# Kernel optimization log

Hardware: AMD Instinct MI355X
Metric: run time of the kernel (lower is better)

Reference implementation:

```python
import jax, jax.numpy as jnp
import numpy as np

D = 256

def setup_inputs() -> dict:
    key = jax.random.key(0)
    ks = jax.random.split(key, 7)
    B, N = 4, 4096
    s = 1.0 / np.sqrt(D)
    return {
        "x": jax.random.normal(ks[0], (B, D, N), dtype=jnp.float32),
        "Wq": jax.random.normal(ks[1], (D, D), dtype=jnp.float32) * s,
        "bq": jax.random.normal(ks[2], (D,), dtype=jnp.float32) * s,
        "Wk": jax.random.normal(ks[3], (D, D), dtype=jnp.float32) * s,
        "bk": jax.random.normal(ks[4], (D,), dtype=jnp.float32) * s,
        "Wv": jax.random.normal(ks[5], (D, D), dtype=jnp.float32) * s,
        "bv": jax.random.normal(ks[6], (D,), dtype=jnp.float32) * s,
    }


def reference(x, Wq, bq, Wk, bk, Wv, bv):
    # x: (B, D, N) -> xt: (B, N, D)
    xt = jnp.swapaxes(x, 1, 2)
    q = xt @ Wq + bq  # (B, N, D)
    k = xt @ Wk + bk
    v = xt @ Wv + bv
    # full N x N attention, NO 1/sqrt(d) scaling (matches original)
    attn = jnp.einsum("bnd,bmd->bnm", q, k)
    attn = jax.nn.softmax(attn, axis=-1)
    out = jnp.einsum("bnm,bmd->bnd", attn, v)  # (B, N, D)
    return jnp.swapaxes(out, 1, 2)  # (B, D, N)
```

## Files before the change

### kernel.cpp

```cpp
#include <hip/hip_runtime.h>
#include <math.h>

#define Dd 256
#define Nn 4096
#define Bb 4
#define BQ 128
#define BK 128
#define SPLIT 2

typedef _Float16 f16;
typedef _Float16 half8 __attribute__((ext_vector_type(8)));
typedef _Float16 half4 __attribute__((ext_vector_type(4)));
typedef float f32x4 __attribute__((ext_vector_type(4)));

#define LOG2E 1.4426950408889634f

template <int CTRL>
__device__ __forceinline__ float dppf(float x) {
    int r = __builtin_amdgcn_update_dpp(0, __builtin_bit_cast(int, x),
                                        CTRL, 0xF, 0xF, false);
    return __builtin_bit_cast(float, r);
}
__device__ __forceinline__ float red16_max(float x) {
    x = fmaxf(x, dppf<0x128>(x));
    x = fmaxf(x, dppf<0x124>(x));
    x = fmaxf(x, dppf<0x122>(x));
    x = fmaxf(x, dppf<0x121>(x));
    return x;
}
__device__ __forceinline__ float red16_sum(float x) {
    x += dppf<0x128>(x); x += dppf<0x124>(x);
    x += dppf<0x122>(x); x += dppf<0x121>(x);
    return x;
}

__global__ __launch_bounds__(256) void wtrans(
    const float* __restrict__ Wq, const float* __restrict__ Wk,
    const float* __restrict__ Wv, f16* __restrict__ Wt)
{
    __shared__ float ld[64][65];
    const int which = blockIdx.y;
    const float* W = which == 0 ? Wq : (which == 1 ? Wk : Wv);
    const int tr = (blockIdx.x >> 2) * 64;
    const int tc = (blockIdx.x & 3) * 64;
    const int t = threadIdx.x;
    #pragma unroll
    for (int i = 0; i < 16; ++i) {
        int u = t + i * 256, r = u >> 6, c = u & 63;
        ld[r][c] = W[(size_t)(tr + r) * Dd + tc + c];
    }
    __syncthreads();
    f16* Wo = Wt + (size_t)which * Dd * Dd;
    #pragma unroll
    for (int i = 0; i < 16; ++i) {
        int u = t + i * 256, cp = u >> 6, rp = u & 63;
        Wo[(size_t)(tc + cp) * Dd + tr + rp] = (f16)ld[rp][cp];
    }
}

__global__ __launch_bounds__(512, 1) void qkv_fused(
    const float* __restrict__ x, const f16* __restrict__ Wt,
    const float* __restrict__ bq, const float* __restrict__ bk,
    const float* __restrict__ bv,
    f16* __restrict__ Qh, f16* __restrict__ Kh, f16* __restrict__ Vth)
{
    __shared__ __align__(16) f16 Ws[256][264];
    __shared__ float bs3[3][256];
    f16 (*xT)[264] = (f16 (*)[264])&Ws[0][0];

    const int t = threadIdx.x;
    const int wave = t >> 6, lane = t & 63, quad = lane >> 4, l15 = lane & 15;
    const int g = wave & 3;
    const int h = wave >> 2;
    const int n0 = blockIdx.x * 64;
    const int b = blockIdx.y;

    if (t < 256) { bs3[0][t] = bq[t]; bs3[1][t] = bk[t]; bs3[2][t] = bv[t]; }

    const float* xb = x + (size_t)b * Dd * Nn;
    #pragma unroll
    for (int i = 0; i < 8; ++i) {
        int u = t + i * 512, d = u >> 4, nq = (u & 15) * 4;
        float4 v4 = *(const float4*)&xb[(size_t)d * Nn + n0 + nq];
        xT[nq + 0][d] = (f16)v4.x; xT[nq + 1][d] = (f16)v4.y;
        xT[nq + 2][d] = (f16)v4.z; xT[nq + 3][d] = (f16)v4.w;
    }
    __syncthreads();

    half8 a[8];
    #pragma unroll
    for (int c = 0; c < 8; ++c)
        a[c] = *(const half8*)&xT[16 * g + l15][c * 32 + quad * 8];

    const int nrow = n0 + 16 * g + quad * 4;

    for (int which = 0; which < 3; ++which) {
        __syncthreads();

        const f16* Wb = Wt + (size_t)which * Dd * Dd;
        #pragma unroll
        for (int i = 0; i < 16; ++i) {
            int u = t + i * 512;
            int r = u >> 5, c = u & 31;
            *(half8*)&Ws[r][c * 8] = *(const half8*)(Wb + (size_t)r * Dd + c * 8);
        }
        __syncthreads();

        f32x4 acc[8];
        #pragma unroll
        for (int dt = 0; dt < 8; ++dt) acc[dt] = (f32x4){0.f, 0.f, 0.f, 0.f};
        #pragma unroll
        for (int c = 0; c < 8; ++c) {
            #pragma unroll
            for (int dt = 0; dt < 8; ++dt) {
                half8 bfr = *(const half8*)&Ws[h * 128 + dt * 16 + l15][c * 32 + quad * 8];
                acc[dt] = __builtin_amdgcn_mfma_f32_16x16x32_f16(a[c], bfr, acc[dt], 0, 0, 0);
            }
        }

        if (which < 2) {
            f16* O = (which == 0 ? Qh : Kh) + ((size_t)b * Nn + nrow) * Dd;
            #pragma unroll
            for (int dt = 0; dt < 8; ++dt) {
                int col = h * 128 + dt * 16 + l15;
                float bvv = bs3[which][col];
                #pragma unroll
                for (int r = 0; r < 4; ++r)
                    O[(size_t)r * Dd + col] = (f16)(acc[dt][r] + bvv);
            }
        } else {
            f16* O = Vth + (size_t)b * Dd * Nn;
            #pragma unroll
            for (int dt = 0; dt < 8; ++dt) {
                int col = h * 128 + dt * 16 + l15;
                float bvv = bs3[2][col];
                half4 o;
                #pragma unroll
                for (int r = 0; r < 4; ++r) o[r] = (f16)(acc[dt][r] + bvv);
                *(half4*)&O[(size_t)col * Nn + nrow] = o;
            }
        }
    }
}

__global__ __launch_bounds__(512, 2) void attn_mfma(
    const f16* __restrict__ Qh, const f16* __restrict__ Kh,
    const f16* __restrict__ Vth, f16* __restrict__ Opart,
    float* __restrict__ mpart, float* __restrict__ lpart)
{
    __shared__ __align__(16) f16 Ks[2][BK][264];
    __shared__ float alpha_s[8][16];
    __shared__ float l_sh[8][16];

    const int t    = threadIdx.x;
    const int wave = t >> 6, lane = t & 63;
    const int quad = lane >> 4, l15 = lane & 15;
    const int b    = blockIdx.y;
    const int s    = blockIdx.z;
    const int q0   = blockIdx.x * BQ;
    const int qw   = q0 + wave * 16;
    const int kvlen = Nn / SPLIT;
    const int kv0  = s * kvlen;

    half8 qf[8];
    const f16* Qrow = Qh + ((size_t)b * Nn + qw + l15) * Dd + quad * 8;
    #pragma unroll
    for (int c = 0; c < 8; ++c) {
        qf[c] = *(const half8*)(Qrow + c * 32);
        qf[c] = qf[c] * (f16)LOG2E;
    }

    f32x4 acc[16];
    #pragma unroll
    for (int n = 0; n < 16; ++n) acc[n] = (f32x4){0.f, 0.f, 0.f, 0.f};
    f32x4 m4 = {-1e30f, -1e30f, -1e30f, -1e30f};
    f32x4 l4 = {0.f, 0.f, 0.f, 0.f};

    const f16* Kb   = Kh + (size_t)b * Nn * Dd;
    const f16* Vrow = Vth + (size_t)b * Dd * Nn
                    + (size_t)(wave * 32 + l15) * Nn + quad * 8;

    #pragma unroll
    for (int i = 0; i < 8; ++i) {
        int u = t + i * 512;
        int r = u >> 5, c = u & 31;
        *(half8*)&Ks[0][r][c * 8] =
            *(const half8*)(Kb + (size_t)(kv0 + r) * Dd + c * 8);
    }
    __syncthreads();

    int buf = 0;
    for (int k0 = kv0; k0 < kv0 + kvlen; k0 += BK) {
        const int kn = k0 + BK;
        const bool havenext = kn < kv0 + kvlen;
        half8 kreg[8];
        if (havenext) {
            #pragma unroll
            for (int i = 0; i < 8; ++i) {
                int u = t + i * 512;
                int r = u >> 5, c = u & 31;
                kreg[i] = *(const half8*)(Kb + (size_t)(kn + r) * Dd + c * 8);
            }
        }

        half8 vbf[2][4];
        #pragma unroll
        for (int dt = 0; dt < 2; ++dt) {
            #pragma unroll
            for (int cbb = 0; cbb < 4; ++cbb)
                vbf[dt][cbb] = *(const half8*)(Vrow + (size_t)dt * 16 * Nn + k0 + cbb * 32);
        }

        f32x4 S[8];
        #pragma unroll
        for (int cb = 0; cb < 8; ++cb) S[cb] = (f32x4){0.f, 0.f, 0.f, 0.f};
        #pragma unroll
        for (int c = 0; c < 8; ++c) {
            #pragma unroll
            for (int cb = 0; cb < 8; ++cb) {
                half8 kb = *(const half8*)&Ks[buf][cb * 16 + l15][c * 32 + quad * 8];
                S[cb] = __builtin_amdgcn_mfma_f32_16x16x32_f16(qf[c], kb, S[cb], 0, 0, 0);
            }
        }

        f32x4 tmax = S[0];
        #pragma unroll
        for (int cb = 1; cb < 8; ++cb) {
            tmax.x = fmaxf(tmax.x, S[cb].x); tmax.y = fmaxf(tmax.y, S[cb].y);
            tmax.z = fmaxf(tmax.z, S[cb].z); tmax.w = fmaxf(tmax.w, S[cb].w);
        }
        tmax.x = red16_max(tmax.x); tmax.y = red16_max(tmax.y);
        tmax.z = red16_max(tmax.z); tmax.w = red16_max(tmax.w);
        f32x4 newm;
        newm.x = fmaxf(m4.x, tmax.x); newm.y = fmaxf(m4.y, tmax.y);
        newm.z = fmaxf(m4.z, tmax.z); newm.w = fmaxf(m4.w, tmax.w);
        f32x4 al;
        al.x = __builtin_amdgcn_exp2f(m4.x - newm.x);
        al.y = __builtin_amdgcn_exp2f(m4.y - newm.y);
        al.z = __builtin_amdgcn_exp2f(m4.z - newm.z);
        al.w = __builtin_amdgcn_exp2f(m4.w - newm.w);
        #pragma unroll
        for (int cb = 0; cb < 8; ++cb) {
            S[cb].x = __builtin_amdgcn_exp2f(S[cb].x - newm.x);
            S[cb].y = __builtin_amdgcn_exp2f(S[cb].y - newm.y);
            S[cb].z = __builtin_amdgcn_exp2f(S[cb].z - newm.z);
            S[cb].w = __builtin_amdgcn_exp2f(S[cb].w - newm.w);
        }
        f32x4 rsum = S[0];
        #pragma unroll
        for (int cb = 1; cb < 8; ++cb) rsum += S[cb];
        rsum.x = red16_sum(rsum.x); rsum.y = red16_sum(rsum.y);
        rsum.z = red16_sum(rsum.z); rsum.w = red16_sum(rsum.w);
        l4 = l4 * al + rsum;
        m4 = newm;

        __syncthreads();

        f16 (*Ps)[16][136] = (f16 (*)[16][136])&Ks[buf][0][0];
        const int pr = quad * 4;
        #pragma unroll
        for (int cb = 0; cb < 8; ++cb) {
            Ps[wave][pr + 0][cb * 16 + l15] = (f16)S[cb].x;
            Ps[wave][pr + 1][cb * 16 + l15] = (f16)S[cb].y;
            Ps[wave][pr + 2][cb * 16 + l15] = (f16)S[cb].z;
            Ps[wave][pr + 3][cb * 16 + l15] = (f16)S[cb].w;
        }
        if (l15 == 0) {
            float4 a4 = {al.x, al.y, al.z, al.w};
            *(float4*)&alpha_s[wave][pr] = a4;
        }
        __syncthreads();

        float4 alq[8];
        int need = 0;
        #pragma unroll
        for (int qb = 0; qb < 8; ++qb) {
            alq[qb] = *(const float4*)&alpha_s[qb][pr];
            need |= (alq[qb].x != 1.f) | (alq[qb].y != 1.f) |
                    (alq[qb].z != 1.f) | (alq[qb].w != 1.f);
        }
        if (__any(need)) {
            #pragma unroll
            for (int qb = 0; qb < 8; ++qb) {
                f32x4 a = {alq[qb].x, alq[qb].y, alq[qb].z, alq[qb].w};
                acc[qb * 2 + 0] *= a;
                acc[qb * 2 + 1] *= a;
            }
        }

        #pragma unroll
        for (int qb = 0; qb < 8; ++qb) {
            #pragma unroll
            for (int cbb = 0; cbb < 4; ++cbb) {
                half8 ap = *(const half8*)&Ps[qb][l15][cbb * 32 + quad * 8];
                acc[qb * 2 + 0] = __builtin_amdgcn_mfma_f32_16x16x32_f16(
                    ap, vbf[0][cbb], acc[qb * 2 + 0], 0, 0, 0);
                acc[qb * 2 + 1] = __builtin_amdgcn_mfma_f32_16x16x32_f16(
                    ap, vbf[1][cbb], acc[qb * 2 + 1], 0, 0, 0);
            }
        }

        if (havenext) {
            #pragma unroll
            for (int i = 0; i < 8; ++i) {
                int u = t + i * 512;
                int r = u >> 5, c = u & 31;
                *(half8*)&Ks[buf ^ 1][r][c * 8] = kreg[i];
            }
            buf ^= 1;
        }
        __syncthreads();
    }

    if (l15 == 0) {
        const int pr = quad * 4;
        float4 lv = {l4.x, l4.y, l4.z, l4.w};
        *(float4*)&l_sh[wave][pr] = lv;
        float mv[4] = {m4.x, m4.y, m4.z, m4.w};
        float lvv[4] = {l4.x, l4.y, l4.z, l4.w};
        #pragma unroll
        for (int r = 0; r < 4; ++r) {
            int n = qw + pr + r;
            mpart[(size_t)(s * Bb + b) * Nn + n] = mv[r];
            lpart[(size_t)(s * Bb + b) * Nn + n] = lvv[r];
        }
    }
    __syncthreads();

    f16* Ob = Opart + (size_t)(s * Bb + b) * Dd * Nn;
    #pragma unroll
    for (int qb = 0; qb < 8; ++qb) {
        float4 lq = *(const float4*)&l_sh[qb][quad * 4];
        f32x4 inv = {1.f / lq.x, 1.f / lq.y, 1.f / lq.z, 1.f / lq.w};
        #pragma unroll
        for (int dt = 0; dt < 2; ++dt) {
            int d = wave * 32 + dt * 16 + l15;
            f32x4 o = acc[qb * 2 + dt] * inv;
            half4 oh;
            oh[0] = (f16)o.x; oh[1] = (f16)o.y; oh[2] = (f16)o.z; oh[3] = (f16)o.w;
            *(half4*)&Ob[(size_t)d * Nn + q0 + qb * 16 + quad * 4] = oh;
        }
    }
}

__global__ __launch_bounds__(256) void combine(
    const f16* __restrict__ Opart, const float* __restrict__ mpart,
    const float* __restrict__ lpart, float* __restrict__ out)
{
    const int t = threadIdx.x;
    const int n0 = (blockIdx.x * 256 + t) * 8;
    const int d = blockIdx.y, b = blockIdx.z;

    float m[SPLIT][8], l[SPLIT][8];
    #pragma unroll
    for (int s = 0; s < SPLIT; ++s) {
        size_t base = (size_t)(s * Bb + b) * Nn + n0;
        float4 a0 = *(const float4*)&mpart[base];
        float4 a1 = *(const float4*)&mpart[base + 4];
        float4 c0 = *(const float4*)&lpart[base];
        float4 c1 = *(const float4*)&lpart[base + 4];
        m[s][0]=a0.x; m[s][1]=a0.y; m[s][2]=a0.z; m[s][3]=a0.w;
        m[s][4]=a1.x; m[s][5]=a1.y; m[s][6]=a1.z; m[s][7]=a1.w;
        l[s][0]=c0.x; l[s][1]=c0.y; l[s][2]=c0.z; l[s][3]=c0.w;
        l[s][4]=c1.x; l[s][5]=c1.y; l[s][6]=c1.z; l[s][7]=c1.w;
    }
    float w[SPLIT][8];
    #pragma unroll
    for (int jx = 0; jx < 8; ++jx) {
        float M = m[0][jx];
        #pragma unroll
        for (int s = 1; s < SPLIT; ++s) M = fmaxf(M, m[s][jx]);
        float L = 0.f;
        #pragma unroll
        for (int s = 0; s < SPLIT; ++s) {
            float ws = l[s][jx] * __builtin_amdgcn_exp2f(m[s][jx] - M);
            w[s][jx] = ws; L += ws;
        }
        float invL = 1.f / L;
        #pragma unroll
        for (int s = 0; s < SPLIT; ++s) w[s][jx] *= invL;
    }

    float o[8];
    #pragma unroll
    for (int jx = 0; jx < 8; ++jx) o[jx] = 0.f;
    #pragma unroll
    for (int s = 0; s < SPLIT; ++s) {
        half8 h = *(const half8*)&Opart[((size_t)(s * Bb + b) * Dd + d) * Nn + n0];
        #pragma unroll
        for (int jx = 0; jx < 8; ++jx) o[jx] += w[s][jx] * (float)h[jx];
    }
    float* op = out + ((size_t)b * Dd + d) * Nn + n0;
    f32x4 o0 = {o[0], o[1], o[2], o[3]};
    f32x4 o1 = {o[4], o[5], o[6], o[7]};
    *(f32x4*)op = o0;
    *(f32x4*)(op + 4) = o1;
}

extern "C" void kernel_launch(void* const* d_in, const int* in_sizes, int n_in,
                              void* d_out, int out_size, void* d_ws, size_t ws_size,
                              hipStream_t stream) {
    const float* x  = (const float*)d_in[0];
    const float* Wq = (const float*)d_in[1];
    const float* bq = (const float*)d_in[2];
    const float* Wk = (const float*)d_in[3];
    const float* bk = (const float*)d_in[4];
    const float* Wv = (const float*)d_in[5];
    const float* bv = (const float*)d_in[6];
    float* out = (float*)d_out;

    f16* Qh    = (f16*)d_ws;
    f16* Kh    = Qh + (size_t)Bb * Nn * Dd;
    f16* Vth   = Kh + (size_t)Bb * Nn * Dd;
    f16* Wt    = Vth + (size_t)Bb * Nn * Dd;
    f16* Opart = Wt + (size_t)3 * Dd * Dd;
    float* mpart = (float*)(Opart + (size_t)SPLIT * Bb * Dd * Nn);
    float* lpart = mpart + (size_t)SPLIT * Bb * Nn;

    wtrans<<<dim3(16, 3), 256, 0, stream>>>(Wq, Wk, Wv, Wt);
    qkv_fused<<<dim3(Nn / 64, Bb), 512, 0, stream>>>(
        x, Wt, bq, bk, bv, Qh, Kh, Vth);
    attn_mfma<<<dim3(Nn / BQ, Bb, SPLIT), 512, 0, stream>>>(
        Qh, Kh, Vth, Opart, mpart, lpart);
    combine<<<dim3(Nn / 2048, Dd, Bb), 256, 0, stream>>>(
        Opart, mpart, lpart, out);
}
```

Baseline: 210.5 us.

## Restructure QKV projection to load weights directly into registers and split output columns

The QKV projection kernel no longer stages each 256x256 weight matrix in shared memory. Each wave now loads its 32-column weight fragments straight from global memory into registers and reads the x tile from a much smaller shared buffer. The grid doubles by splitting output columns across two blocks with 256 threads each, which cuts shared memory use and removes the per-projection barriers, so more blocks can be resident. In exchange, x is loaded twice per tile, weights are read from global memory (likely served from L2) with more register pressure, and the attention kernel, which dominates the runtime, is unchanged.

```diff
diff --git a/kernel.cpp b/kernel.cpp
--- a/kernel.cpp
+++ b/kernel.cpp
@@ -58,86 +58,95 @@
     }
 }
 
-__global__ __launch_bounds__(512, 1) void qkv_fused(
+__global__ __launch_bounds__(256) void qkv_fused(
     const float* __restrict__ x, const f16* __restrict__ Wt,
     const float* __restrict__ bq, const float* __restrict__ bk,
     const float* __restrict__ bv,
     f16* __restrict__ Qh, f16* __restrict__ Kh, f16* __restrict__ Vth)
 {
-    __shared__ __align__(16) f16 Ws[256][264];
-    __shared__ float bs3[3][256];
-    f16 (*xT)[264] = (f16 (*)[264])&Ws[0][0];
+    __shared__ __align__(16) f16 xT[64][264];
 
     const int t = threadIdx.x;
     const int wave = t >> 6, lane = t & 63, quad = lane >> 4, l15 = lane & 15;
-    const int g = wave & 3;
-    const int h = wave >> 2;
-    const int n0 = blockIdx.x * 64;
-    const int b = blockIdx.y;
-
-    if (t < 256) { bs3[0][t] = bq[t]; bs3[1][t] = bk[t]; bs3[2][t] = bv[t]; }
+    const int n0  = blockIdx.x * 64;
+    const int ch  = blockIdx.y;
+    const int b   = blockIdx.z;
+    const int col0 = ch * 128 + wave * 32;
 
     const float* xb = x + (size_t)b * Dd * Nn;
     #pragma unroll
-    for (int i = 0; i < 8; ++i) {
-        int u = t + i * 512, d = u >> 4, nq = (u & 15) * 4;
+    for (int i = 0; i < 16; ++i) {
+        int u = t + i * 256, d = u >> 4, nq = (u & 15) * 4;
         float4 v4 = *(const float4*)&xb[(size_t)d * Nn + n0 + nq];
         xT[nq + 0][d] = (f16)v4.x; xT[nq + 1][d] = (f16)v4.y;
         xT[nq + 2][d] = (f16)v4.z; xT[nq + 3][d] = (f16)v4.w;
     }
+
+    float bias[3][2];
+    #pragma unroll
+    for (int ct = 0; ct < 2; ++ct) {
+        int col = col0 + ct * 16 + l15;
+        bias[0][ct] = bq[col]; bias[1][ct] = bk[col]; bias[2][ct] = bv[col];
+    }
+
     __syncthreads();
 
-    half8 a[8];
-    #pragma unroll
-    for (int c = 0; c < 8; ++c)
-        a[c] = *(const half8*)&xT[16 * g + l15][c * 32 + quad * 8];
-
-    const int nrow = n0 + 16 * g + quad * 4;
-
+    #pragma unroll
     for (int which = 0; which < 3; ++which) {
-        __syncthreads();
-
         const f16* Wb = Wt + (size_t)which * Dd * Dd;
-        #pragma unroll
-        for (int i = 0; i < 16; ++i) {
-            int u = t + i * 512;
-            int r = u >> 5, c = u & 31;
-            *(half8*)&Ws[r][c * 8] = *(const half8*)(Wb + (size_t)r * Dd + c * 8);
-        }
-        __syncthreads();
-
-        f32x4 acc[8];
-        #pragma unroll
-        for (int dt = 0; dt < 8; ++dt) acc[dt] = (f32x4){0.f, 0.f, 0.f, 0.f};
-        #pragma unroll
-        for (int c = 0; c < 8; ++c) {
-            #pragma unroll
-            for (int dt = 0; dt < 8; ++dt) {
-                half8 bfr = *(const half8*)&Ws[h * 128 + dt * 16 + l15][c * 32 + quad * 8];
-                acc[dt] = __builtin_amdgcn_mfma_f32_16x16x32_f16(a[c], bfr, acc[dt], 0, 0, 0);
+        half8 wf[2][8];
+        #pragma unroll
+        for (int ct = 0; ct < 2; ++ct)
+            #pragma unroll
+            for (int c = 0; c < 8; ++c)
+                wf[ct][c] = *(const half8*)(Wb
+                    + (size_t)(col0 + ct * 16 + l15) * Dd + c * 32 + quad * 8);
+
+        f32x4 acc[4][2];
+        #pragma unroll
+        for (int rg = 0; rg < 4; ++rg) {
+            acc[rg][0] = (f32x4){0.f, 0.f, 0.f, 0.f};
+            acc[rg][1] = (f32x4){0.f, 0.f, 0.f, 0.f};
+        }
+        #pragma unroll
+        for (int rg = 0; rg < 4; ++rg) {
+            #pragma unroll
+            for (int c = 0; c < 8; ++c) {
+                half8 a = *(const half8*)&xT[rg * 16 + l15][c * 32 + quad * 8];
+                acc[rg][0] = __builtin_amdgcn_mfma_f32_16x16x32_f16(
+                    a, wf[0][c], acc[rg][0], 0, 0, 0);
+                acc[rg][1] = __builtin_amdgcn_mfma_f32_16x16x32_f16(
+                    a, wf[1][c], acc[rg][1], 0, 0, 0);
             }
         }
 
         if (which < 2) {
-            f16* O = (which == 0 ? Qh : Kh) + ((size_t)b * Nn + nrow) * Dd;
-            #pragma unroll
-            for (int dt = 0; dt < 8; ++dt) {
-                int col = h * 128 + dt * 16 + l15;
-                float bvv = bs3[which][col];
+            f16* O = (which == 0 ? Qh : Kh) + ((size_t)b * Nn + n0) * Dd;
+            #pragma unroll
+            for (int rg = 0; rg < 4; ++rg) {
                 #pragma unroll
-                for (int r = 0; r < 4; ++r)
-                    O[(size_t)r * Dd + col] = (f16)(acc[dt][r] + bvv);
+                for (int ct = 0; ct < 2; ++ct) {
+                    int col = col0 + ct * 16 + l15;
+                    float bvv = bias[which][ct];
+                    #pragma unroll
+                    for (int r = 0; r < 4; ++r)
+                        O[(size_t)(rg * 16 + quad * 4 + r) * Dd + col] =
+                            (f16)(acc[rg][ct][r] + bvv);
+                }
             }
         } else {
             f16* O = Vth + (size_t)b * Dd * Nn;
             #pragma unroll
-            for (int dt = 0; dt < 8; ++dt) {
-                int col = h * 128 + dt * 16 + l15;
-                float bvv = bs3[2][col];
-                half4 o;
+            for (int rg = 0; rg < 4; ++rg) {
                 #pragma unroll
-                for (int r = 0; r < 4; ++r) o[r] = (f16)(acc[dt][r] + bvv);
-                *(half4*)&O[(size_t)col * Nn + nrow] = o;
+                for (int ct = 0; ct < 2; ++ct) {
+                    int col = col0 + ct * 16 + l15;
+                    float bvv = bias[2][ct];
+                    half4 o;
+                    #pragma unroll
+                    for (int r = 0; r < 4; ++r) o[r] = (f16)(acc[rg][ct][r] + bvv);
+                    *(half4*)&O[(size_t)col * Nn + n0 + rg * 16 + quad * 4] = o;
+                }
             }
         }
     }
@@ -418,7 +427,7 @@
     float* lpart = mpart + (size_t)SPLIT * Bb * Nn;
 
     wtrans<<<dim3(16, 3), 256, 0, stream>>>(Wq, Wk, Wv, Wt);
-    qkv_fused<<<dim3(Nn / 64, Bb), 512, 0, stream>>>(
+    qkv_fused<<<dim3(Nn / 64, 2, Bb), 256, 0, stream>>>(
         x, Wt, bq, bk, bv, Qh, Kh, Vth);
     attn_mfma<<<dim3(Nn / BQ, Bb, SPLIT), 512, 0, stream>>>(
         Qh, Kh, Vth, Opart, mpart, lpart);
```

Measured after the change: 209.4 us. No clear change (-0.5%).
